# Kernel tuning notes

Hardware: AMD Instinct MI355X
Metric: run time of the kernel (lower is better)

Reference implementation:

```python
import jax, jax.numpy as jnp
import numpy as np

KH, KW = 3, 3
STRIDE = (1, 1)
PAD = ((1, 1), (1, 1))
WEIGHT_BIT = 8


def asym_quant_params(num_bits, smin, smax):
    # ZeroQ asymmetric_linear_quantization_params (signed, integral zero point)
    n = 2.0 ** num_bits - 1.0
    scale = n / jnp.maximum(smax - smin, 1e-8)
    zero_point = jnp.round(scale * smin) + 2.0 ** (num_bits - 1)
    return scale, zero_point


def setup_inputs() -> dict:
    key = jax.random.key(0)
    k1, k2, k3 = jax.random.split(key, 3)
    x = jax.random.normal(k1, (16, 128, 56, 56), dtype=jnp.float32)
    weight = jax.random.normal(k2, (128, 128, 3, 3), dtype=jnp.float32) * 0.05
    bias = jax.random.normal(k3, (128,), dtype=jnp.float32) * 0.1
    return {"x": x, "weight": weight, "bias": bias, "activation_bit": 8}


def reference(x, weight, bias, activation_bit):
    B, C, H, W = x.shape
    Cout = weight.shape[0]

    # nn.functional.unfold(x, 3, stride=1, padding=1).transpose(1, 2)
    # conv_general_dilated_patches emits feature dim ordered (c, kh, kw),
    # matching torch unfold's channel-major layout.
    patches = jax.lax.conv_general_dilated_patches(
        x, filter_shape=(KH, KW), window_strides=STRIDE, padding=PAD)
    _, F, OH, OW = patches.shape          # F = C*KH*KW
    L = OH * OW
    calc_x = patches.reshape(B, F, L).transpose(0, 2, 1)  # [B, L, F]

    # ----- weight quantization: per-output-channel asymmetric int8 -----
    w2 = weight.reshape(Cout, -1)                          # [Cout, F]
    w_min = w2.min(axis=1)
    w_max = w2.max(axis=1)
    scale_w, zp_w = asym_quant_params(WEIGHT_BIT, w_min, w_max)  # [Cout]
    nw = 2.0 ** (WEIGHT_BIT - 1)
    qw = jnp.clip(jnp.round(scale_w[:, None] * w2 - zp_w[:, None]), -nw, nw - 1)

    # ----- activation quantization: per-tensor asymmetric -----
    x_min = calc_x.min()
    x_max = calc_x.max()
    scale_x, zp_x = asym_quant_params(activation_bit, x_min, x_max)
    nx = 2.0 ** (activation_bit - 1)
    qx = jnp.clip(jnp.round(scale_x * calc_x - zp_x), -nx, nx - 1)  # [B, L, F]

    # bias: linear_quantize(bias, scale_w*scale_x, 0)
    qb = jnp.round(scale_w * scale_x * bias)                # [Cout]

    # integer matmul + asymmetric zero-point correction
    # real value r ~= (q + zp) / scale, so
    # x.w*sx*sw = qx.qw + zp_w*sum(qx) + zp_x*sum(qw) + K*zp_w*zp_x
    mult_res = jnp.einsum('blf,of->blo', qx, qw)            # [B, L, Cout]
    K = w2.shape[1]
    res = (mult_res
           + zp_w * qx.sum(-1, keepdims=True)               # [B, L, 1]*[Cout]
           + zp_x * qw.sum(axis=1)                          # [Cout]
           + K * zp_w * zp_x
           + qb)                                            # [B, L, Cout]

    # requantize accumulator to activation_bit bits, then dequantize
    r_min, r_max = res.min(), res.max()
    scale_r, zp_r = asym_quant_params(activation_bit, r_min, r_max)
    nr = 2.0 ** (activation_bit - 1)
    qr = jnp.clip(jnp.round(scale_r * res - zp_r), -nr, nr - 1)
    out = (qr + zp_r) / scale_r / (scale_w * scale_x)       # [B, L, Cout]

    return out.transpose(0, 2, 1)                           # [B, Cout, L]
```

## Files before the change

### kernel.cpp

```cpp
#include <hip/hip_runtime.h>
#include <hip/hip_cooperative_groups.h>
#include <stdint.h>

#pragma clang fp contract(off)

namespace cg = cooperative_groups;

typedef __attribute__((ext_vector_type(4))) int i32x4;
typedef __attribute__((ext_vector_type(16))) int i32x16;

#define B_    16
#define C_    128
#define HW_   56
#define L_    3136
#define CO_   128
#define F_    1152
#define M_    50176
#define NT_   784

#define OFF_PBMIN 0
#define OFF_PBMAX 3136
#define OFF_PRMIN 6272
#define OFF_PRMAX 9408
#define OFF_SW    12544
#define OFF_ZPW   13056
#define OFF_CT    13568
#define OFF_QW    16384
#define OFF_QX    163840
#define OFF_S     6586368
#define OFF_RES   6787072

__device__ __forceinline__ int read_abit(const int* p) {
    int i = *p;
    if (i > 0 && i < 32) return i;
    float f = __int_as_float(i);
    int fi = (int)f;
    return (fi > 0 && fi < 32) ? fi : 8;
}

__device__ __forceinline__ int swz_tile(int blk) {
    return (blk & 7) * 98 + (blk >> 3);
}

__device__ __forceinline__ void block_fminmax(float& mn, float& mx, float* sred) {
    for (int m = 32; m; m >>= 1) {
        mn = fminf(mn, __shfl_xor(mn, m));
        mx = fmaxf(mx, __shfl_xor(mx, m));
    }
    int w = threadIdx.x >> 6;
    if ((threadIdx.x & 63) == 0) { sred[w] = mn; sred[4 + w] = mx; }
    __syncthreads();
    mn = fminf(fminf(sred[0], sred[1]), fminf(sred[2], sred[3]));
    mx = fmaxf(fmaxf(sred[4], sred[5]), fmaxf(sred[6], sred[7]));
    __syncthreads();
}
__device__ __forceinline__ void block_iminmax(int& mn, int& mx, int* ired) {
    for (int m = 32; m; m >>= 1) {
        mn = min(mn, __shfl_xor(mn, m));
        mx = max(mx, __shfl_xor(mx, m));
    }
    int w = threadIdx.x >> 6;
    if ((threadIdx.x & 63) == 0) { ired[w] = mn; ired[4 + w] = mx; }
    __syncthreads();
    mn = min(min(ired[0], ired[1]), min(ired[2], ired[3]));
    mx = max(max(ired[4], ired[5]), max(ired[6], ired[7]));
    __syncthreads();
}
__device__ __forceinline__ int block_isum(int v, int* ired) {
    for (int m = 32; m; m >>= 1) v += __shfl_xor(v, m);
    int w = threadIdx.x >> 6;
    if ((threadIdx.x & 63) == 0) ired[w] = v;
    __syncthreads();
    v = ired[0] + ired[1] + ired[2] + ired[3];
    __syncthreads();
    return v;
}

__device__ __forceinline__ void dev_p1(const float4* __restrict__ x4, int n4,
                                       char* ws, float* sred) {
    float mn = 0.0f, mx = 0.0f;
    int stride = gridDim.x * blockDim.x;
    for (int i = blockIdx.x * blockDim.x + threadIdx.x; i < n4; i += stride) {
        float4 v = x4[i];
        mn = fminf(mn, fminf(fminf(v.x, v.y), fminf(v.z, v.w)));
        mx = fmaxf(mx, fmaxf(fmaxf(v.x, v.y), fmaxf(v.z, v.w)));
    }
    block_fminmax(mn, mx, sred);
    if (threadIdx.x == 0) {
        ((float*)(ws + OFF_PBMIN))[blockIdx.x] = mn;
        ((float*)(ws + OFF_PBMAX))[blockIdx.x] = mx;
    }
}

__device__ __forceinline__ void dev_reduce_pb(const char* ws, float* sred,
                                              float& xmin, float& xmax) {
    const float* pbmin = (const float*)(ws + OFF_PBMIN);
    const float* pbmax = (const float*)(ws + OFF_PBMAX);
    float mn = 0.0f, mx = 0.0f;
    for (int i = threadIdx.x; i < NT_; i += 256) {
        mn = fminf(mn, pbmin[i]);
        mx = fmaxf(mx, pbmax[i]);
    }
    block_fminmax(mn, mx, sred);
    xmin = mn; xmax = mx;
}

__device__ __forceinline__ void dev_reduce_pr(const char* ws, int* ired,
                                              int& rmin, int& rmax) {
    const int* prmin = (const int*)(ws + OFF_PRMIN);
    const int* prmax = (const int*)(ws + OFF_PRMAX);
    int mn = INT32_MAX, mx = INT32_MIN;
    for (int i = threadIdx.x; i < NT_; i += 256) {
        mn = min(mn, prmin[i]);
        mx = max(mx, prmax[i]);
    }
    block_iminmax(mn, mx, ired);
    rmin = mn; rmax = mx;
}

__device__ __forceinline__ void dev_p2x(const float* __restrict__ x, char* ws, char* pool,
                                        float sx, float zx, int nx) {
    int (*ssum)[64] = (int(*)[64])pool;
    float lo = -(float)nx, hif = (float)(nx - 1);
    signed char* qxt = (signed char*)(ws + OFF_QX);
    int gid = swz_tile(blockIdx.x);
    int b = gid / 49, lcq = gid - b * 49;
    int l0 = lcq * 64;
    int t = threadIdx.x, lane = t & 63, cgp = t >> 6;
    int l = l0 + lane;
    const float* xb = x + ((size_t)b * C_) * L_ + l;
    int4* dst = (int4*)(qxt + ((size_t)(b * L_ + l)) * 128);
    int psum = 0;
    #pragma unroll
    for (int ii = 0; ii < 2; ++ii) {
        int c16 = (cgp + 4 * ii) * 16;
        int wds[4];
        #pragma unroll
        for (int k = 0; k < 4; ++k) {
            int wv = 0;
            #pragma unroll
            for (int e = 0; e < 4; ++e) {
                int c = c16 + 4 * k + e;
                float v = xb[(size_t)c * L_];
                int qi = (int)fminf(fmaxf(rintf(sx * v - zx), lo), hif);
                psum += qi;
                wv |= (qi & 255) << (8 * e);
            }
            wds[k] = wv;
        }
        int4 vv; vv.x = wds[0]; vv.y = wds[1]; vv.z = wds[2]; vv.w = wds[3];
        dst[c16 >> 4] = vv;
    }
    ssum[cgp][lane] = psum;
    __syncthreads();
    if (cgp == 0) {
        int* S = (int*)(ws + OFF_S);
        S[b * L_ + l] = ssum[0][lane] + ssum[1][lane] + ssum[2][lane] + ssum[3][lane];
    }
    __syncthreads();
}

__device__ __forceinline__ void dev_p2w(const float* __restrict__ wgt,
                                        const float* __restrict__ bias,
                                        char* ws, float* sred, int* ired,
                                        float sx, float zx) {
    int o = blockIdx.x;
    const float* wr = wgt + o * F_;
    float mn = 3.4e38f, mx = -3.4e38f;
    for (int f = threadIdx.x; f < F_; f += 256) {
        float v = wr[f];
        mn = fminf(mn, v); mx = fmaxf(mx, v);
    }
    block_fminmax(mn, mx, sred);
    float sw = 255.0f / fmaxf(mx - mn, 1e-8f);
    float zw = rintf(sw * mn) + 128.0f;
    signed char* qw = (signed char*)(ws + OFF_QW);
    int qsum = 0;
    for (int f = threadIdx.x; f < F_; f += 256) {
        float q = fminf(fmaxf(rintf(sw * wr[f] - zw), -128.0f), 127.0f);
        int qi = (int)q;
        qsum += qi;
        int c = f / 9, j = f - c * 9;
        qw[j * 16384 + (c >> 4) * 2048 + (o << 4) + (c & 15)] = (signed char)qi;
    }
    qsum = block_isum(qsum, ired);
    if (threadIdx.x == 0) {
        float qb = rintf(sw * sx * bias[o]);
        int zwi = (int)zw, zxi = (int)zx;
        ((int*)(ws + OFF_CT))[o] = zxi * qsum + F_ * zwi * zxi + (int)qb;
        ((int*)(ws + OFF_ZPW))[o] = zwi;
        ((float*)(ws + OFF_SW))[o] = sw;
    }
}

template <bool WRITE_RES>
__device__ __forceinline__ void dev_p3(char* __restrict__ ws, char* pool, int* ired,
                                       int abit, float sx, float zx,
                                       i32x16& acc0, i32x16& acc1) {
    signed char* As = (signed char*)pool;
    signed char* Bs = (signed char*)(pool + 8192);
    int* S_s = (int*)(pool + 24576);
    int* sq  = (int*)(pool + 25504);
    const signed char* qxt = (const signed char*)(ws + OFF_QX);
    const signed char* qw  = (const signed char*)(ws + OFF_QW);
    const int* Sg  = (const int*)(ws + OFF_S);
    const int* zpw = (const int*)(ws + OFF_ZPW);
    const int* ct  = (const int*)(ws + OFF_CT);

    int t = threadIdx.x;
    int mg = swz_tile(blockIdx.x) * 64;
    int b = mg / L_, l0 = mg - b * L_;
    int prow0 = l0 / HW_;
    int nx = 1 << (abit - 1);
    int q0 = min(max(-(int)zx, -nx), nx - 1);
    int pw = (q0 & 255) * 0x01010101;
    int4 pad4; pad4.x = pw; pad4.y = pw; pad4.z = pw; pad4.w = pw;
    int padS = C_ * q0;
    const signed char* qxtb = qxt + (size_t)b * L_ * 128;
    const int* Sb = Sg + b * L_;

    int chA = t & 7, rowA0 = t >> 3, rowA1 = rowA0 + 32;
    int li0 = l0 + rowA0, li1 = l0 + rowA1;
    int oh0 = li0 / HW_, ow0 = li0 - oh0 * HW_;
    int oh1 = li1 / HW_, ow1 = li1 - oh1 * HW_;

    int4 a0, a1, br0, br1, br2, br3;
    #define P3_LOAD_A(J) do {                                                          \
        int kh = (J) / 3 - 1, kw = (J) % 3 - 1;                                        \
        int ih = oh0 + kh, iw = ow0 + kw;                                              \
        a0 = ((unsigned)ih < HW_ && (unsigned)iw < HW_)                                \
             ? *(const int4*)(qxtb + ((ih * HW_ + iw) << 7) + (chA << 4)) : pad4;      \
        ih = oh1 + kh; iw = ow1 + kw;                                                  \
        a1 = ((unsigned)ih < HW_ && (unsigned)iw < HW_)                                \
             ? *(const int4*)(qxtb + ((ih * HW_ + iw) << 7) + (chA << 4)) : pad4;      \
    } while (0)
    #define P3_LOAD_B(J) do {                                                          \
        const int4* src = (const int4*)(qw + (J) * 16384);                             \
        br0 = src[t]; br1 = src[256 + t]; br2 = src[512 + t]; br3 = src[768 + t];      \
    } while (0)

    P3_LOAD_A(0); P3_LOAD_B(0);
    if (t < 232) {
        int ri = t / 58, c1 = t - ri * 58;
        int ih = prow0 - 1 + ri, iw = c1 - 1;
        S_s[t] = ((unsigned)ih < HW_ && (unsigned)iw < HW_) ? Sb[ih * HW_ + iw] : padS;
    }
    __syncthreads();
    if (t < 64) {
        int l = l0 + t;
        int oh = l / HW_, ow = l - oh * HW_;
        int ri = oh - prow0 + 1, ci = ow + 1;
        int s = 0;
        #pragma unroll
        for (int dr = -1; dr <= 1; ++dr)
            #pragma unroll
            for (int dc = -1; dc <= 1; ++dc)
                s += S_s[(ri + dr) * 58 + ci + dc];
        sq[t] = s;
    }

    int lane = t & 63, w = t >> 6;
    int wm = (w >> 1) << 5, wn = (w & 1) << 6;
    int r = lane & 31, hi = lane >> 5;
    #pragma unroll
    for (int i = 0; i < 16; ++i) { acc0[i] = 0; acc1[i] = 0; }

    #pragma unroll
    for (int j = 0; j < 9; ++j) {
        if (j > 0) __syncthreads();
        *(int4*)&As[(rowA0 << 7) + ((chA ^ (rowA0 & 7)) << 4)] = a0;
        *(int4*)&As[(rowA1 << 7) + ((chA ^ (rowA1 & 7)) << 4)] = a1;
        {
            int4* d = (int4*)Bs;
            d[t] = br0; d[256 + t] = br1; d[512 + t] = br2; d[768 + t] = br3;
        }
        if (j < 8) { P3_LOAD_A(j + 1); P3_LOAD_B(j + 1); }
        __syncthreads();
        i32x4 af[4], bf0[4], bf1[4];
        #pragma unroll
        for (int kk = 0; kk < 4; ++kk) {
            int ch2 = kk * 2 + hi, row = wm + r;
            af[kk]  = *(const i32x4*)&As[(row << 7) + ((ch2 ^ (row & 7)) << 4)];
            bf0[kk] = *(const i32x4*)&Bs[ch2 * 2048 + ((wn + r) << 4)];
            bf1[kk] = *(const i32x4*)&Bs[ch2 * 2048 + ((wn + 32 + r) << 4)];
        }
        #pragma unroll
        for (int kk = 0; kk < 4; ++kk) {
            acc0 = __builtin_amdgcn_mfma_i32_32x32x32_i8(af[kk], bf0[kk], acc0, 0, 0, 0);
            acc1 = __builtin_amdgcn_mfma_i32_32x32x32_i8(af[kk], bf1[kk], acc1, 0, 0, 0);
        }
    }
    #undef P3_LOAD_A
    #undef P3_LOAD_B

    int o0 = wn + r, o1 = wn + 32 + r;
    int zw0 = zpw[o0], c0 = ct[o0];
    int zw1 = zpw[o1], c1 = ct[o1];
    int lmin = INT32_MAX, lmax = INT32_MIN;
    int* resp = (int*)(ws + OFF_RES);
    #pragma unroll
    for (int g = 0; g < 16; ++g) {
        int row = wm + (g & 3) + ((g >> 2) << 3) + (hi << 2);
        int s = sq[row];
        int v0 = acc0[g] + zw0 * s + c0;
        int v1 = acc1[g] + zw1 * s + c1;
        acc0[g] = v0; acc1[g] = v1;
        lmin = min(lmin, min(v0, v1));
        lmax = max(lmax, max(v0, v1));
        if (WRITE_RES) {
            int m = mg + row;
            resp[m * CO_ + o0] = v0;
            resp[m * CO_ + o1] = v1;
        }
    }
    block_iminmax(lmin, lmax, ired);
    if (t == 0) {
        ((int*)(ws + OFF_PRMIN))[blockIdx.x] = lmin;
        ((int*)(ws + OFF_PRMAX))[blockIdx.x] = lmax;
    }
    __syncthreads();
}

__device__ __forceinline__ void dev_p4(const char* ws, char* pool, float* __restrict__ out,
                                       int abit, float sx, int rmin, int rmax,
                                       const i32x16& acc0, const i32x16& acc1) {
    const float* scale_w = (const float*)(ws + OFF_SW);
    float* tile = (float*)pool;
    int t = threadIdx.x;
    int mg = swz_tile(blockIdx.x) * 64;
    int b = mg / L_, l0 = mg - b * L_;
    int lane = t & 63, w = t >> 6;
    int wm = (w >> 1) << 5, wn = (w & 1) << 6;
    int r = lane & 31, hi = lane >> 5;
    int o0 = wn + r, o1 = wn + 32 + r;
    int nx = 1 << (abit - 1);
    float nlev = (float)((1 << abit) - 1);
    float rminf = (float)rmin, rmaxf = (float)rmax;
    float sr = nlev / fmaxf(rmaxf - rminf, 1e-8f);
    float zr = rintf(sr * rminf) + (float)nx;
    float lo = -(float)nx, hiq = (float)(nx - 1);
    float swsx0 = scale_w[o0] * sx, swsx1 = scale_w[o1] * sx;
    #pragma unroll
    for (int g = 0; g < 16; ++g) {
        int row = wm + (g & 3) + ((g >> 2) << 3) + (hi << 2);
        float qa = fminf(fmaxf(rintf(sr * (float)acc0[g] - zr), lo), hiq);
        float qb = fminf(fmaxf(rintf(sr * (float)acc1[g] - zr), lo), hiq);
        tile[row * 129 + o0] = ((qa + zr) / sr) / swsx0;
        tile[row * 129 + o1] = ((qb + zr) / sr) / swsx1;
    }
    __syncthreads();
    #pragma unroll
    for (int i = 0; i < 8; ++i) {
        int o = (t >> 4) + i * 16;
        int l4 = (t & 15) * 4;
        float4 f;
        #pragma unroll
        for (int jj = 0; jj < 4; ++jj)
            ((float*)&f)[jj] = tile[(l4 + jj) * 129 + o];
        *(float4*)(out + ((size_t)(b * CO_ + o)) * L_ + l0 + l4) = f;
    }
}

__global__ __launch_bounds__(256, 4) void k_fused(const float* __restrict__ x,
                                                  const float* __restrict__ wgt,
                                                  const float* __restrict__ bias,
                                                  const int* __restrict__ abit_p,
                                                  char* __restrict__ ws,
                                                  float* __restrict__ out) {
    __shared__ __align__(16) char pool[33280];
    __shared__ float sred[8];
    __shared__ int ired[8];

    int n4 = (B_ * C_ * L_) / 4;
    dev_p1((const float4*)x, n4, ws, sred);
    cg::this_grid().sync();

    float xmin, xmax;
    dev_reduce_pb(ws, sred, xmin, xmax);
    int abit = read_abit(abit_p);
    float nlv = (float)((1 << abit) - 1);
    float sx = nlv / fmaxf(xmax - xmin, 1e-8f);
    float zx = rintf(sx * xmin) + (float)(1 << (abit - 1));
    int nx = 1 << (abit - 1);
    dev_p2x(x, ws, pool, sx, zx, nx);
    if (blockIdx.x < CO_) dev_p2w(wgt, bias, ws, sred, ired, sx, zx);
    cg::this_grid().sync();

    i32x16 acc0, acc1;
    dev_p3<false>(ws, pool, ired, abit, sx, zx, acc0, acc1);
    cg::this_grid().sync();

    int rmin, rmax;
    dev_reduce_pr(ws, ired, rmin, rmax);
    dev_p4(ws, pool, out, abit, sx, rmin, rmax, acc0, acc1);
}

__global__ __launch_bounds__(256) void fb_p1(const float4* __restrict__ x4, int n4,
                                             char* __restrict__ ws) {
    __shared__ float sred[8];
    dev_p1(x4, n4, ws, sred);
}

__global__ __launch_bounds__(256) void fb_p2(const float* __restrict__ x,
                                             const float* __restrict__ wgt,
                                             const float* __restrict__ bias,
                                             const int* __restrict__ abit_p,
                                             char* __restrict__ ws) {
    __shared__ __align__(16) char pool[1024];
    __shared__ float sred[8];
    __shared__ int ired[8];
    float xmin, xmax;
    dev_reduce_pb(ws, sred, xmin, xmax);
    int abit = read_abit(abit_p);
    float nlv = (float)((1 << abit) - 1);
    float sx = nlv / fmaxf(xmax - xmin, 1e-8f);
    float zx = rintf(sx * xmin) + (float)(1 << (abit - 1));
    int nx = 1 << (abit - 1);
    dev_p2x(x, ws, pool, sx, zx, nx);
    if (blockIdx.x < CO_) dev_p2w(wgt, bias, ws, sred, ired, sx, zx);
}

__global__ __launch_bounds__(256, 4) void fb_p3(const int* __restrict__ abit_p,
                                                char* __restrict__ ws) {
    __shared__ __align__(16) char pool[25760];
    __shared__ float sred[8];
    __shared__ int ired[8];
    float xmin, xmax;
    dev_reduce_pb(ws, sred, xmin, xmax);
    int abit = read_abit(abit_p);
    float nlv = (float)((1 << abit) - 1);
    float sx = nlv / fmaxf(xmax - xmin, 1e-8f);
    float zx = rintf(sx * xmin) + (float)(1 << (abit - 1));
    i32x16 acc0, acc1;
    dev_p3<true>(ws, pool, ired, abit, sx, zx, acc0, acc1);
}

__global__ __launch_bounds__(256) void fb_p4(const int* __restrict__ abit_p,
                                             char* __restrict__ ws,
                                             float* __restrict__ out) {
    __shared__ int tile[64 * 65];
    __shared__ float sred[8];
    __shared__ int ired[8];
    float xmin, xmax;
    dev_reduce_pb(ws, sred, xmin, xmax);
    int abit = read_abit(abit_p);
    float nlv = (float)((1 << abit) - 1);
    float sxv = nlv / fmaxf(xmax - xmin, 1e-8f);
    int rmin, rmax;
    dev_reduce_pr(ws, ired, rmin, rmax);

    const int* res = (const int*)(ws + OFF_RES);
    const float* scale_w = (const float*)(ws + OFF_SW);
    int t = threadIdx.x;
    int bid = blockIdx.x;
    int lcq = bid % 49; int tmp2 = bid / 49; int ocq = tmp2 & 1; int b = tmp2 >> 1;
    int l0 = lcq * 64, o0 = ocq * 64;

    const int* resb = res + ((size_t)(b * L_ + l0)) * CO_ + o0;
    #pragma unroll
    for (int i = 0; i < 4; ++i) {
        int lr = (t >> 4) + i * 16;
        int oc4 = (t & 15) * 4;
        int4 v = *(const int4*)(resb + lr * CO_ + oc4);
        int* d = &tile[lr * 65 + oc4];
        d[0] = v.x; d[1] = v.y; d[2] = v.z; d[3] = v.w;
    }
    int nxq = 1 << (abit - 1);
    float rminf = (float)rmin, rmaxf = (float)rmax;
    float sr = nlv / fmaxf(rmaxf - rminf, 1e-8f);
    float zr = rintf(sr * rminf) + (float)nxq;
    float lo = -(float)nxq, hiq = (float)(nxq - 1);
    __syncthreads();
    #pragma unroll
    for (int i = 0; i < 4; ++i) {
        int o = (t >> 4) + i * 16;
        int l4 = (t & 15) * 4;
        float swsx = scale_w[o0 + o] * sxv;
        float4 f;
        #pragma unroll
        for (int jj = 0; jj < 4; ++jj) {
            int rv = tile[(l4 + jj) * 65 + o];
            float q = fminf(fmaxf(rintf(sr * (float)rv - zr), lo), hiq);
            ((float*)&f)[jj] = ((q + zr) / sr) / swsx;
        }
        *(float4*)(out + ((size_t)(b * CO_ + o0 + o)) * L_ + l0 + l4) = f;
    }
}


extern "C" void kernel_launch(void* const* d_in, const int* in_sizes, int n_in,
                              void* d_out, int out_size, void* d_ws, size_t ws_size,
                              hipStream_t stream) {
    const float* x      = (const float*)d_in[0];
    const float* weight = (const float*)d_in[1];
    const float* bias   = (const float*)d_in[2];
    const int*   abit   = (const int*)d_in[3];
    float* out = (float*)d_out;
    char* ws = (char*)d_ws;

    int dev = 0;
    hipGetDevice(&dev);
    int ncu = 0;
    hipDeviceGetAttribute(&ncu, hipDeviceAttributeMultiprocessorCount, dev);
    int nb = 0;
    hipOccupancyMaxActiveBlocksPerMultiprocessor(&nb, (const void*)k_fused, 256, 0);

    if (nb > 0 && (long)nb * (long)ncu >= NT_) {
        void* args[] = {(void*)&x, (void*)&weight, (void*)&bias,
                        (void*)&abit, (void*)&ws, (void*)&out};
        hipLaunchCooperativeKernel((const void*)k_fused, dim3(NT_), dim3(256),
                                   args, 0, stream);
    } else {
        int n4 = (B_ * C_ * L_) / 4;
        fb_p1<<<NT_, 256, 0, stream>>>((const float4*)x, n4, ws);
        fb_p2<<<NT_, 256, 0, stream>>>(x, weight, bias, abit, ws);
        fb_p3<<<NT_, 256, 0, stream>>>(abit, ws);
        fb_p4<<<1568, 256, 0, stream>>>(abit, ws, out);
    }
}
```

Measured before the change: 57.91 us.

## Replace cooperative grid sync with sharded atomic barrier and move weight quant earlier

Swaps cg::this_grid().sync() for a custom grid barrier that uses 8 counters, each padded onto its own cache line. A memset before the launch zeroes the counters. Weight quantization moves into phase 1 so it overlaps the activation min/max scan, and the bias and zero-point constant is now computed in the GEMM epilogue from the stored qsum. The intent is a cheaper barrier and a better-balanced phase 2, at the cost of an extra memset launch and a spin-wait that assumes all blocks are co-resident.

```diff
diff --git a/kernel.cpp b/kernel.cpp
--- a/kernel.cpp
+++ b/kernel.cpp
@@ -1,10 +1,7 @@
 #include <hip/hip_runtime.h>
-#include <hip/hip_cooperative_groups.h>
 #include <stdint.h>
 
 #pragma clang fp contract(off)
-
-namespace cg = cooperative_groups;
 
 typedef __attribute__((ext_vector_type(4))) int i32x4;
 typedef __attribute__((ext_vector_type(16))) int i32x16;
@@ -24,7 +21,8 @@
 #define OFF_PRMAX 9408
 #define OFF_SW    12544
 #define OFF_ZPW   13056
-#define OFF_CT    13568
+#define OFF_CNT   14080
+#define OFF_QS    15616
 #define OFF_QW    16384
 #define OFF_QX    163840
 #define OFF_S     6586368
@@ -40,6 +38,22 @@
 
 __device__ __forceinline__ int swz_tile(int blk) {
     return (blk & 7) * 98 + (blk >> 3);
+}
+
+__device__ __forceinline__ void gsync(char* ws, int sp) {
+    unsigned* base = (unsigned*)(ws + OFF_CNT) + sp * 128;
+    __syncthreads();
+    if (threadIdx.x == 0) {
+        __threadfence();
+        atomicAdd(&base[(blockIdx.x & 7) * 16], 1u);
+    }
+    if (threadIdx.x < 8) {
+        while (__hip_atomic_load(&base[threadIdx.x * 16],
+                                 __ATOMIC_RELAXED, __HIP_MEMORY_SCOPE_AGENT) < 98u)
+            __builtin_amdgcn_s_sleep(2);
+    }
+    __threadfence();
+    __syncthreads();
 }
 
 __device__ __forceinline__ void block_fminmax(float& mn, float& mx, float* sred) {
@@ -89,6 +103,35 @@
     if (threadIdx.x == 0) {
         ((float*)(ws + OFF_PBMIN))[blockIdx.x] = mn;
         ((float*)(ws + OFF_PBMAX))[blockIdx.x] = mx;
+    }
+}
+
+__device__ __forceinline__ void dev_p1w(const float* __restrict__ wgt,
+                                        char* ws, float* sred, int* ired) {
+    int o = blockIdx.x;
+    const float* wr = wgt + o * F_;
+    float mn = 3.4e38f, mx = -3.4e38f;
+    for (int f = threadIdx.x; f < F_; f += 256) {
+        float v = wr[f];
+        mn = fminf(mn, v); mx = fmaxf(mx, v);
+    }
+    block_fminmax(mn, mx, sred);
+    float sw = 255.0f / fmaxf(mx - mn, 1e-8f);
+    float zw = rintf(sw * mn) + 128.0f;
+    signed char* qw = (signed char*)(ws + OFF_QW);
+    int qsum = 0;
+    for (int f = threadIdx.x; f < F_; f += 256) {
+        float q = fminf(fmaxf(rintf(sw * wr[f] - zw), -128.0f), 127.0f);
+        int qi = (int)q;
+        qsum += qi;
+        int c = f / 9, j = f - c * 9;
+        qw[j * 16384 + (c >> 4) * 2048 + (o << 4) + (c & 15)] = (signed char)qi;
+    }
+    qsum = block_isum(qsum, ired);
+    if (threadIdx.x == 0) {
+        ((int*)(ws + OFF_QS))[o]  = qsum;
+        ((int*)(ws + OFF_ZPW))[o] = (int)zw;
+        ((float*)(ws + OFF_SW))[o] = sw;
     }
 }
 
@@ -160,41 +203,9 @@
     __syncthreads();
 }
 
-__device__ __forceinline__ void dev_p2w(const float* __restrict__ wgt,
-                                        const float* __restrict__ bias,
-                                        char* ws, float* sred, int* ired,
-                                        float sx, float zx) {
-    int o = blockIdx.x;
-    const float* wr = wgt + o * F_;
-    float mn = 3.4e38f, mx = -3.4e38f;
-    for (int f = threadIdx.x; f < F_; f += 256) {
-        float v = wr[f];
-        mn = fminf(mn, v); mx = fmaxf(mx, v);
-    }
-    block_fminmax(mn, mx, sred);
-    float sw = 255.0f / fmaxf(mx - mn, 1e-8f);
-    float zw = rintf(sw * mn) + 128.0f;
-    signed char* qw = (signed char*)(ws + OFF_QW);
-    int qsum = 0;
-    for (int f = threadIdx.x; f < F_; f += 256) {
-        float q = fminf(fmaxf(rintf(sw * wr[f] - zw), -128.0f), 127.0f);
-        int qi = (int)q;
-        qsum += qi;
-        int c = f / 9, j = f - c * 9;
-        qw[j * 16384 + (c >> 4) * 2048 + (o << 4) + (c & 15)] = (signed char)qi;
-    }
-    qsum = block_isum(qsum, ired);
-    if (threadIdx.x == 0) {
-        float qb = rintf(sw * sx * bias[o]);
-        int zwi = (int)zw, zxi = (int)zx;
-        ((int*)(ws + OFF_CT))[o] = zxi * qsum + F_ * zwi * zxi + (int)qb;
-        ((int*)(ws + OFF_ZPW))[o] = zwi;
-        ((float*)(ws + OFF_SW))[o] = sw;
-    }
-}
-
 template <bool WRITE_RES>
 __device__ __forceinline__ void dev_p3(char* __restrict__ ws, char* pool, int* ired,
+                                       const float* __restrict__ bias,
                                        int abit, float sx, float zx,
                                        i32x16& acc0, i32x16& acc1) {
     signed char* As = (signed char*)pool;
@@ -205,7 +216,6 @@
     const signed char* qw  = (const signed char*)(ws + OFF_QW);
     const int* Sg  = (const int*)(ws + OFF_S);
     const int* zpw = (const int*)(ws + OFF_ZPW);
-    const int* ct  = (const int*)(ws + OFF_CT);
 
     int t = threadIdx.x;
     int mg = swz_tile(blockIdx.x) * 64;
@@ -294,8 +304,12 @@
     #undef P3_LOAD_B
 
     int o0 = wn + r, o1 = wn + 32 + r;
-    int zw0 = zpw[o0], c0 = ct[o0];
-    int zw1 = zpw[o1], c1 = ct[o1];
+    const int* qs = (const int*)(ws + OFF_QS);
+    const float* swp = (const float*)(ws + OFF_SW);
+    int zxi = (int)zx;
+    int zw0 = zpw[o0], zw1 = zpw[o1];
+    int c0 = zxi * qs[o0] + F_ * zw0 * zxi + (int)rintf(swp[o0] * sx * bias[o0]);
+    int c1 = zxi * qs[o1] + F_ * zw1 * zxi + (int)rintf(swp[o1] * sx * bias[o1]);
     int lmin = INT32_MAX, lmax = INT32_MIN;
     int* resp = (int*)(ws + OFF_RES);
     #pragma unroll
@@ -373,7 +387,8 @@
 
     int n4 = (B_ * C_ * L_) / 4;
     dev_p1((const float4*)x, n4, ws, sred);
-    cg::this_grid().sync();
+    if (blockIdx.x < CO_) dev_p1w(wgt, ws, sred, ired);
+    gsync(ws, 0);
 
     float xmin, xmax;
     dev_reduce_pb(ws, sred, xmin, xmax);
@@ -383,12 +398,11 @@
     float zx = rintf(sx * xmin) + (float)(1 << (abit - 1));
     int nx = 1 << (abit - 1);
     dev_p2x(x, ws, pool, sx, zx, nx);
-    if (blockIdx.x < CO_) dev_p2w(wgt, bias, ws, sred, ired, sx, zx);
-    cg::this_grid().sync();
+    gsync(ws, 1);
 
     i32x16 acc0, acc1;
-    dev_p3<false>(ws, pool, ired, abit, sx, zx, acc0, acc1);
-    cg::this_grid().sync();
+    dev_p3<false>(ws, pool, ired, bias, abit, sx, zx, acc0, acc1);
+    gsync(ws, 2);
 
     int rmin, rmax;
     dev_reduce_pr(ws, ired, rmin, rmax);
@@ -396,19 +410,19 @@
 }
 
 __global__ __launch_bounds__(256) void fb_p1(const float4* __restrict__ x4, int n4,
+                                             const float* __restrict__ wgt,
                                              char* __restrict__ ws) {
     __shared__ float sred[8];
+    __shared__ int ired[8];
     dev_p1(x4, n4, ws, sred);
+    if (blockIdx.x < CO_) dev_p1w(wgt, ws, sred, ired);
 }
 
 __global__ __launch_bounds__(256) void fb_p2(const float* __restrict__ x,
-                                             const float* __restrict__ wgt,
-                                             const float* __restrict__ bias,
                                              const int* __restrict__ abit_p,
                                              char* __restrict__ ws) {
     __shared__ __align__(16) char pool[1024];
     __shared__ float sred[8];
-    __shared__ int ired[8];
     float xmin, xmax;
     dev_reduce_pb(ws, sred, xmin, xmax);
     int abit = read_abit(abit_p);
@@ -417,10 +431,10 @@
     float zx = rintf(sx * xmin) + (float)(1 << (abit - 1));
     int nx = 1 << (abit - 1);
     dev_p2x(x, ws, pool, sx, zx, nx);
-    if (blockIdx.x < CO_) dev_p2w(wgt, bias, ws, sred, ired, sx, zx);
-}
-
-__global__ __launch_bounds__(256, 4) void fb_p3(const int* __restrict__ abit_p,
+}
+
+__global__ __launch_bounds__(256, 4) void fb_p3(const float* __restrict__ bias,
+                                                const int* __restrict__ abit_p,
                                                 char* __restrict__ ws) {
     __shared__ __align__(16) char pool[25760];
     __shared__ float sred[8];
@@ -432,7 +446,7 @@
     float sx = nlv / fmaxf(xmax - xmin, 1e-8f);
     float zx = rintf(sx * xmin) + (float)(1 << (abit - 1));
     i32x16 acc0, acc1;
-    dev_p3<true>(ws, pool, ired, abit, sx, zx, acc0, acc1);
+    dev_p3<true>(ws, pool, ired, bias, abit, sx, zx, acc0, acc1);
 }
 
 __global__ __launch_bounds__(256) void fb_p4(const int* __restrict__ abit_p,
@@ -506,15 +520,16 @@
     hipOccupancyMaxActiveBlocksPerMultiprocessor(&nb, (const void*)k_fused, 256, 0);
 
     if (nb > 0 && (long)nb * (long)ncu >= NT_) {
+        hipMemsetAsync(ws + OFF_CNT, 0, 1536, stream);
         void* args[] = {(void*)&x, (void*)&weight, (void*)&bias,
                         (void*)&abit, (void*)&ws, (void*)&out};
         hipLaunchCooperativeKernel((const void*)k_fused, dim3(NT_), dim3(256),
                                    args, 0, stream);
     } else {
         int n4 = (B_ * C_ * L_) / 4;
-        fb_p1<<<NT_, 256, 0, stream>>>((const float4*)x, n4, ws);
-        fb_p2<<<NT_, 256, 0, stream>>>(x, weight, bias, abit, ws);
-        fb_p3<<<NT_, 256, 0, stream>>>(abit, ws);
+        fb_p1<<<NT_, 256, 0, stream>>>((const float4*)x, n4, weight, ws);
+        fb_p2<<<NT_, 256, 0, stream>>>(x, abit, ws);
+        fb_p3<<<NT_, 256, 0, stream>>>(bias, abit, ws);
         fb_p4<<<1568, 256, 0, stream>>>(abit, ws, out);
     }
 }
```

Result: no change. 58.24 us (+0.6%).
